# Performance work log

Measured on AMD Instinct MI355X. Metric: run time of the kernel, lower is better.

## Reference

```python
import jax, jax.numpy as jnp
import numpy as np

B = 16384
NUM_DENSE = 13
NUM_SPARSE = 26
VOCAB = 100000
EMB = 64
MLP_DIMS = [512, 256, 64]
TOP_OUT = 256
TRIU_I, TRIU_J = np.triu_indices(NUM_SPARSE, k=1)  # 325 pairs


def setup_inputs() -> dict:
    key = jax.random.key(0)
    ks = jax.random.split(key, 12)
    inp = {}
    inp["dense_features"] = jax.random.normal(ks[0], (B, NUM_DENSE), dtype=jnp.float32)
    inp["sparse_features"] = jax.random.randint(ks[1], (B, NUM_SPARSE), 0, VOCAB, dtype=jnp.int64)
    # embedding tables, all same shape -> stacked [F, V, D]
    inp["tables"] = jax.random.normal(ks[2], (NUM_SPARSE, VOCAB, EMB), dtype=jnp.float32) * 0.01
    # bottom (dense) MLP: 13 -> 512 -> 256 -> 64, weights stored [in, out]
    dims = [NUM_DENSE] + MLP_DIMS
    for li in range(3):
        fan_in = dims[li]
        inp[f"W{li}"] = jax.random.normal(ks[3 + li], (dims[li], dims[li + 1]), dtype=jnp.float32) / np.sqrt(fan_in)
        inp[f"b{li}"] = jnp.zeros((dims[li + 1],), dtype=jnp.float32)
    # top MLP: (64 + 325) -> 256
    top_in = MLP_DIMS[-1] + NUM_SPARSE * (NUM_SPARSE - 1) // 2
    inp["Wt"] = jax.random.normal(ks[6], (top_in, TOP_OUT), dtype=jnp.float32) / np.sqrt(top_in)
    inp["bt"] = jnp.zeros((TOP_OUT,), dtype=jnp.float32)
    return inp


def reference(dense_features, sparse_features, tables, W0, b0, W1, b1, W2, b2, Wt, bt):
    # bottom MLP with ReLU after every layer (as in the torch Sequential)
    x = jax.nn.relu(dense_features @ W0 + b0)
    x = jax.nn.relu(x @ W1 + b1)
    dense_out = jax.nn.relu(x @ W2 + b2)  # [B, 64]

    # embedding gather: table f indexed by sparse_features[:, f] -> [B, F, D]
    emb = jax.vmap(lambda t, idx: t[idx], in_axes=(0, 1), out_axes=1)(tables, sparse_features)

    # pairwise dot interaction, upper triangle (i < j) -> [B, 325]
    gram = jnp.einsum('bid,bjd->bij', emb, emb)
    interact = gram[:, TRIU_I, TRIU_J]

    features = jnp.concatenate([dense_out, interact], axis=1)  # [B, 389]
    return features @ Wt + bt  # [B, 256]
```

## Files before the change

kernel.cpp:

```cpp
#include <hip/hip_runtime.h>
#include <hip/hip_bf16.h>


#define BATCH   16384
#define NSPARSE 26
#define VOCAB   100000
#define EMB     64
#define KTOP    416
#define KREAL   389
#define SPB     32
#define ASTR    424
#define X1STR   520
#define X2STR   264

typedef __attribute__((ext_vector_type(8)))  short bf16x8;
typedef __attribute__((ext_vector_type(4)))  short s16x4;
typedef __attribute__((ext_vector_type(4)))  float f32x4;
typedef __attribute__((ext_vector_type(16))) float f32x16;

__device__ inline void gload_lds16(const void* g, void* l) {
    __builtin_amdgcn_global_load_lds(
        (const __attribute__((address_space(1))) void*)g,
        (__attribute__((address_space(3))) void*)l, 16, 0, 0);
}

__device__ inline short f2bf(float x) {
    __hip_bfloat16 h = __float2bfloat16(x);
    return *reinterpret_cast<short*>(&h);
}

__global__ __launch_bounds__(256)
void prep_weights(const float* __restrict__ W0, const float* __restrict__ W1,
                  const float* __restrict__ W2, const float* __restrict__ Wt,
                  short* __restrict__ W0t, short* __restrict__ W1t,
                  short* __restrict__ W2t, short* __restrict__ Wtt)
{
    __shared__ float tile[32][36];
    int b = blockIdx.x, t = threadIdx.x;
    const float* src; short* dst; int K, N, Kpad, k0, n0;
    if (b < 16)        {              src = W0; dst = W0t; K = 13;  N = 512; Kpad = 32;  k0 = 0;           n0 = b * 32; }
    else if (b < 144)  { int i = b - 16;  src = W1; dst = W1t; K = 512; N = 256; Kpad = 512; k0 = (i >> 3) * 32; n0 = (i & 7) * 32; }
    else if (b < 160)  { int i = b - 144; src = W2; dst = W2t; K = 256; N = 64;  Kpad = 256; k0 = (i >> 1) * 32; n0 = (i & 1) * 32; }
    else               { int i = b - 160; src = Wt; dst = Wtt; K = 389; N = 256; Kpad = 416; k0 = (i >> 3) * 32; n0 = (i & 7) * 32; }

    int r = t >> 3, c4 = (t & 7) * 4;
    int gr = k0 + r;
    float4 v = make_float4(0.f, 0.f, 0.f, 0.f);
    if (gr < K) v = *(const float4*)(src + (size_t)gr * N + n0 + c4);
    tile[r][c4 + 0] = v.x; tile[r][c4 + 1] = v.y;
    tile[r][c4 + 2] = v.z; tile[r][c4 + 3] = v.w;
    __syncthreads();
    s16x4 o;
    #pragma unroll
    for (int j = 0; j < 4; ++j) o[j] = f2bf(tile[c4 + j][r]);
    *(s16x4*)&dst[(size_t)(n0 + r) * Kpad + k0 + c4] = o;
}

__global__ __launch_bounds__(256, 2)
void fused_all(const int* __restrict__ sparse, const float* __restrict__ tables,
               const float* __restrict__ D,
               const short* __restrict__ W0t, const float* __restrict__ b0,
               const short* __restrict__ W1t, const float* __restrict__ b1,
               const short* __restrict__ W2t, const float* __restrict__ b2,
               const short* __restrict__ Wtt, const float* __restrict__ bt,
               float* __restrict__ out)
{
    __shared__ __align__(16) char smem[78848];
    short* As  = (short*)(smem);
    short* X1s = (short*)(smem + 27136);
    short* X2s = (short*)(smem + 27136);
    short* Bst = (short*)(smem + 60416);
    short* Ds  = (short*)(smem + 76800);

    int tid = threadIdx.x;
    int w = tid >> 6, lane = tid & 63;
    int lr = lane & 15, lg = lane >> 4;
    int wr = w >> 1, wc = w & 1;
    int swz = (lg ^ (lr & 3)) * 8;
    int sbase = blockIdx.x * SPB;

    for (int x = tid; x < SPB * 13; x += 256) {
        int r = x / 13, k = x - r * 13;
        Ds[r * 32 + k] = f2bf(D[(size_t)sbase * 13 + x]);
    }
    for (int x = tid; x < SPB * 19; x += 256) {
        int r = x / 19, k = 13 + (x - r * 19);
        Ds[r * 32 + k] = 0;
    }
    for (int x = tid; x < SPB * 27; x += 256) {
        int r = x / 27, c = x - r * 27;
        As[r * ASTR + KREAL + c] = 0;
    }
    __syncthreads();

    auto gram_phase = [&]() {
        int row = lane & 31, half = lane >> 5;
        int srow = (row < NSPARSE) ? row : 0;
        int idxv[8];
        #pragma unroll
        for (int li = 0; li < 8; ++li)
            idxv[li] = sparse[(sbase + w * 8 + li) * NSPARSE + srow];

        f32x4 Ca[4], Cb[4], Na[4], Nb[4];
        {
            const float* rp = tables + ((long)srow * VOCAB + idxv[0]) * EMB + half * 8;
            #pragma unroll
            for (int t = 0; t < 4; ++t) {
                Ca[t] = *(const f32x4*)(rp + t * 16);
                Cb[t] = *(const f32x4*)(rp + t * 16 + 4);
            }
        }
        #pragma unroll
        for (int li = 0; li < 8; ++li) {
            if (li < 7) {
                const float* rp = tables + ((long)srow * VOCAB + idxv[li + 1]) * EMB + half * 8;
                #pragma unroll
                for (int t = 0; t < 4; ++t) {
                    Na[t] = *(const f32x4*)(rp + t * 16);
                    Nb[t] = *(const f32x4*)(rp + t * 16 + 4);
                }
            }
            f32x16 acc = {};
            #pragma unroll
            for (int t = 0; t < 4; ++t) {
                bf16x8 f;
                #pragma unroll
                for (int j = 0; j < 4; ++j) f[j] = f2bf(Ca[t][j]);
                #pragma unroll
                for (int j = 0; j < 4; ++j) f[4 + j] = f2bf(Cb[t][j]);
                acc = __builtin_amdgcn_mfma_f32_32x32x16_bf16(f, f, acc, 0, 0, 0);
            }
            int c = row;
            if (c < NSPARSE) {
                #pragma unroll
                for (int reg = 0; reg < 16; ++reg) {
                    int r = (reg & 3) + 8 * (reg >> 2) + 4 * half;
                    if (r < c) {
                        int p = r * (2 * NSPARSE - r - 1) / 2 + (c - r - 1);
                        As[(w * 8 + li) * ASTR + 64 + p] = f2bf(acc[reg]);
                    }
                }
            }
            #pragma unroll
            for (int t = 0; t < 4; ++t) { Ca[t] = Na[t]; Cb[t] = Nb[t]; }
        }
    };

    auto mlp_phase = [&]() {
        {
            bf16x8 a = *(const bf16x8*)&Ds[(wr * 16 + lr) * 32 + lg * 8];
            f32x4 acc[16] = {};
            #pragma unroll
            for (int ni = 0; ni < 16; ++ni) {
                bf16x8 b = *(const bf16x8*)(W0t + (size_t)(wc * 256 + ni * 16 + lr) * 32 + lg * 8);
                acc[ni] = __builtin_amdgcn_mfma_f32_16x16x32_bf16(a, b, acc[ni], 0, 0, 0);
            }
            #pragma unroll
            for (int ni = 0; ni < 16; ++ni) {
                int col = wc * 256 + ni * 16 + lr;
                float bv = b0[col];
                #pragma unroll
                for (int j = 0; j < 4; ++j) {
                    int r = wr * 16 + lg * 4 + j;
                    X1s[r * X1STR + col] = f2bf(fmaxf(acc[ni][j] + bv, 0.f));
                }
            }
        }
        {
            f32x4 acc[8] = {};
            for (int k0 = 0; k0 < 512; k0 += 32) {
                #pragma unroll
                for (int rd = 0; rd < 4; ++rd) {
                    int slot = rd * 256 + tid;
                    int n = slot >> 2, kc = slot & 3;
                    gload_lds16(W1t + (size_t)n * 512 + k0 + (kc ^ (n & 3)) * 8, &Bst[slot * 8]);
                }
                __syncthreads();
                bf16x8 a = *(const bf16x8*)&X1s[(wr * 16 + lr) * X1STR + k0 + lg * 8];
                #pragma unroll
                for (int ni = 0; ni < 8; ++ni) {
                    int n = wc * 128 + ni * 16 + lr;
                    bf16x8 b = *(const bf16x8*)&Bst[n * 32 + swz];
                    acc[ni] = __builtin_amdgcn_mfma_f32_16x16x32_bf16(a, b, acc[ni], 0, 0, 0);
                }
                __syncthreads();
            }
            #pragma unroll
            for (int ni = 0; ni < 8; ++ni) {
                int col = wc * 128 + ni * 16 + lr;
                float bv = b1[col];
                #pragma unroll
                for (int j = 0; j < 4; ++j) {
                    int r = wr * 16 + lg * 4 + j;
                    X2s[r * X2STR + col] = f2bf(fmaxf(acc[ni][j] + bv, 0.f));
                }
            }
        }
        {
            f32x4 acc[2] = {};
            for (int k0 = 0; k0 < 256; k0 += 32) {
                {
                    int n = tid >> 2, kc = tid & 3;
                    gload_lds16(W2t + (size_t)n * 256 + k0 + (kc ^ (n & 3)) * 8, &Bst[tid * 8]);
                }
                __syncthreads();
                bf16x8 a = *(const bf16x8*)&X2s[(wr * 16 + lr) * X2STR + k0 + lg * 8];
                #pragma unroll
                for (int ni = 0; ni < 2; ++ni) {
                    int n = wc * 32 + ni * 16 + lr;
                    bf16x8 b = *(const bf16x8*)&Bst[n * 32 + swz];
                    acc[ni] = __builtin_amdgcn_mfma_f32_16x16x32_bf16(a, b, acc[ni], 0, 0, 0);
                }
                __syncthreads();
            }
            #pragma unroll
            for (int ni = 0; ni < 2; ++ni) {
                int col = wc * 32 + ni * 16 + lr;
                float bv = b2[col];
                #pragma unroll
                for (int j = 0; j < 4; ++j) {
                    int r = wr * 16 + lg * 4 + j;
                    As[r * ASTR + col] = f2bf(fmaxf(acc[ni][j] + bv, 0.f));
                }
            }
        }
    };

    if ((blockIdx.x >> 8) & 1) { mlp_phase(); gram_phase(); }
    else                       { gram_phase(); mlp_phase(); }

    {
        f32x4 acc[8] = {};
        for (int k0 = 0; k0 < KTOP; k0 += 32) {
            #pragma unroll
            for (int rd = 0; rd < 4; ++rd) {
                int slot = rd * 256 + tid;
                int n = slot >> 2, kc = slot & 3;
                gload_lds16(Wtt + (size_t)n * KTOP + k0 + (kc ^ (n & 3)) * 8, &Bst[slot * 8]);
            }
            __syncthreads();
            bf16x8 a = *(const bf16x8*)&As[(wr * 16 + lr) * ASTR + k0 + lg * 8];
            #pragma unroll
            for (int ni = 0; ni < 8; ++ni) {
                int n = wc * 128 + ni * 16 + lr;
                bf16x8 b = *(const bf16x8*)&Bst[n * 32 + swz];
                acc[ni] = __builtin_amdgcn_mfma_f32_16x16x32_bf16(a, b, acc[ni], 0, 0, 0);
            }
            __syncthreads();
        }
        #pragma unroll
        for (int ni = 0; ni < 8; ++ni) {
            int col = wc * 128 + ni * 16 + lr;
            float bv = bt[col];
            #pragma unroll
            for (int j = 0; j < 4; ++j) {
                int r = wr * 16 + lg * 4 + j;
                out[(size_t)(sbase + r) * 256 + col] = acc[ni][j] + bv;
            }
        }
    }
}

extern "C" void kernel_launch(void* const* d_in, const int* in_sizes, int n_in,
                              void* d_out, int out_size, void* d_ws, size_t ws_size,
                              hipStream_t stream)
{
    const float* dense  = (const float*)d_in[0];
    const int*   sparse = (const int*)  d_in[1];
    const float* tables = (const float*)d_in[2];
    const float* W0     = (const float*)d_in[3];
    const float* b0     = (const float*)d_in[4];
    const float* W1     = (const float*)d_in[5];
    const float* b1     = (const float*)d_in[6];
    const float* W2     = (const float*)d_in[7];
    const float* b2     = (const float*)d_in[8];
    const float* Wt     = (const float*)d_in[9];
    const float* bt     = (const float*)d_in[10];
    float* out = (float*)d_out;

    char* ws = (char*)d_ws;
    short* W0t = (short*)(ws);
    short* W1t = (short*)(ws + 32768);
    short* W2t = (short*)(ws + 294912);
    short* Wtt = (short*)(ws + 327680);

    prep_weights<<<264, 256, 0, stream>>>(W0, W1, W2, Wt, W0t, W1t, W2t, Wtt);

    fused_all<<<BATCH / SPB, 256, 0, stream>>>(sparse, tables, dense,
                                               W0t, b0, W1t, b1, W2t, b2,
                                               Wtt, bt, out);
}
```

Measured before the change: 52.03 us.

## Warp-specialize fused kernel: MLP waves overlap gather-gram waves, 64 samples per block

Moves from 256-thread blocks of 32 samples, where every wave ran the MLP and gram phases in sequence, to 512-thread blocks of 64 samples. Four waves run the bottom MLP while the other four gather embeddings and compute the gram interactions, so the MLP compute overlaps the gather latency. Each MLP wave now stages its own slice of the weights with its own waits instead of a block-wide barrier. LDS uses an XOR swizzle in place of padded strides, and the top GEMM double-buffers its weight tiles. The cost is one block per CU with about 156KB of LDS, and the gram work is split into 2/10/4-sample chunks to match the MLP stages, which may leave the two wave groups unbalanced.

```diff
diff --git a/kernel.cpp b/kernel.cpp
--- a/kernel.cpp
+++ b/kernel.cpp
@@ -5,13 +5,13 @@
 #define BATCH   16384
 #define NSPARSE 26
 #define VOCAB   100000
-#define EMB     64
 #define KTOP    416
 #define KREAL   389
-#define SPB     32
-#define ASTR    424
-#define X1STR   520
-#define X2STR   264
+#define SPB     64
+
+#define WAIT_VMCNT(N) asm volatile("s_waitcnt vmcnt(" #N ")" ::: "memory")
+#define WAIT_LGKM0()  asm volatile("s_waitcnt lgkmcnt(0)" ::: "memory")
+#define SBAR0() __builtin_amdgcn_sched_barrier(0)
 
 typedef __attribute__((ext_vector_type(8)))  short bf16x8;
 typedef __attribute__((ext_vector_type(4)))  short s16x4;
@@ -27,6 +27,19 @@
 __device__ inline short f2bf(float x) {
     __hip_bfloat16 h = __float2bfloat16(x);
     return *reinterpret_cast<short*>(&h);
+}
+
+__device__ inline f32x4 mfma16(bf16x8 a, bf16x8 b, f32x4 c) {
+    return __builtin_amdgcn_mfma_f32_16x16x32_bf16(a, b, c, 0, 0, 0);
+}
+
+__device__ inline short* ldsx2(char* base, int row, int ld, int col) {
+    int byte = ((row * ld + col) * 2) ^ ((row & 7) << 4);
+    return (short*)(base + byte);
+}
+__device__ inline bf16x8 ldsx16(const char* base, int row, int ld, int col) {
+    int byte = ((row * ld + col) * 2) ^ ((row & 7) << 4);
+    return *(const bf16x8*)(base + byte);
 }
 
 __global__ __launch_bounds__(256)
@@ -56,7 +69,63 @@
     *(s16x4*)&dst[(size_t)(n0 + r) * Kpad + k0 + c4] = o;
 }
 
-__global__ __launch_bounds__(256, 2)
+template<int CNT>
+__device__ void gram_run(int s0, int gw, int sbase,
+                         const int* __restrict__ sparse,
+                         const float* __restrict__ tables,
+                         char* AsG, int lane)
+{
+    int row = lane & 31, half = lane >> 5;
+    int srow = (row < NSPARSE) ? row : 0;
+    int sl0 = gw * 16 + s0;
+
+    const float* rp0 = tables + ((long)srow * VOCAB +
+        sparse[(sbase + sl0) * NSPARSE + srow]) * 64 + half * 8;
+    f32x4 Ca[4], Cb[4], Na[4], Nb[4];
+    #pragma unroll
+    for (int t = 0; t < 4; ++t) {
+        Ca[t] = *(const f32x4*)(rp0 + t * 16);
+        Cb[t] = *(const f32x4*)(rp0 + t * 16 + 4);
+    }
+    #pragma unroll
+    for (int li = 0; li < CNT; ++li) {
+        if (li + 1 < CNT) {
+            const float* rp = tables + ((long)srow * VOCAB +
+                sparse[(sbase + sl0 + li + 1) * NSPARSE + srow]) * 64 + half * 8;
+            #pragma unroll
+            for (int t = 0; t < 4; ++t) {
+                Na[t] = *(const f32x4*)(rp + t * 16);
+                Nb[t] = *(const f32x4*)(rp + t * 16 + 4);
+            }
+        }
+        f32x16 acc = {};
+        #pragma unroll
+        for (int t = 0; t < 4; ++t) {
+            bf16x8 f;
+            #pragma unroll
+            for (int j = 0; j < 4; ++j) f[j] = f2bf(Ca[t][j]);
+            #pragma unroll
+            for (int j = 0; j < 4; ++j) f[4 + j] = f2bf(Cb[t][j]);
+            acc = __builtin_amdgcn_mfma_f32_32x32x16_bf16(f, f, acc, 0, 0, 0);
+        }
+        int c = row, sl = sl0 + li;
+        if (c < NSPARSE) {
+            #pragma unroll
+            for (int reg = 0; reg < 16; ++reg) {
+                int r = (reg & 3) + 8 * (reg >> 2) + 4 * half;
+                if (r < c) {
+                    int p = r * (2 * NSPARSE - r - 1) / 2 + (c - r - 1);
+                    int byte = ((sl * 352 + p) * 2) ^ ((sl & 7) << 4);
+                    *(short*)(AsG + byte) = f2bf(acc[reg]);
+                }
+            }
+        }
+        #pragma unroll
+        for (int t = 0; t < 4; ++t) { Ca[t] = Na[t]; Cb[t] = Nb[t]; }
+    }
+}
+
+__global__ __launch_bounds__(512, 1)
 void fused_all(const int* __restrict__ sparse, const float* __restrict__ tables,
                const float* __restrict__ D,
                const short* __restrict__ W0t, const float* __restrict__ b0,
@@ -65,198 +134,186 @@
                const short* __restrict__ Wtt, const float* __restrict__ bt,
                float* __restrict__ out)
 {
-    __shared__ __align__(16) char smem[78848];
-    short* As  = (short*)(smem);
-    short* X1s = (short*)(smem + 27136);
-    short* X2s = (short*)(smem + 27136);
-    short* Bst = (short*)(smem + 60416);
-    short* Ds  = (short*)(smem + 76800);
+    __shared__ __align__(16) char smem[159744];
+    char* X1s  = smem;
+    char* AsD  = smem;
+    char* X2s  = smem + 65536;
+    char* AsG  = smem + 98304;
+    char* wbuf = smem + 143360;
 
     int tid = threadIdx.x;
     int w = tid >> 6, lane = tid & 63;
     int lr = lane & 15, lg = lane >> 4;
-    int wr = w >> 1, wc = w & 1;
-    int swz = (lg ^ (lr & 3)) * 8;
+    int swz8 = (lg ^ (lr & 3)) * 8;
     int sbase = blockIdx.x * SPB;
-
-    for (int x = tid; x < SPB * 13; x += 256) {
-        int r = x / 13, k = x - r * 13;
-        Ds[r * 32 + k] = f2bf(D[(size_t)sbase * 13 + x]);
-    }
-    for (int x = tid; x < SPB * 19; x += 256) {
-        int r = x / 19, k = 13 + (x - r * 19);
-        Ds[r * 32 + k] = 0;
-    }
-    for (int x = tid; x < SPB * 27; x += 256) {
-        int r = x / 27, c = x - r * 27;
-        As[r * ASTR + KREAL + c] = 0;
+    bool mlp = (w < 4);
+
+    if (mlp) {
+        bf16x8 a[4];
+        #pragma unroll
+        for (int mi = 0; mi < 4; ++mi) {
+            bf16x8 t = {};
+            if (lg < 2) {
+                #pragma unroll
+                for (int j = 0; j < 8; ++j) {
+                    int k = lg * 8 + j;
+                    if (k < 13)
+                        t[j] = f2bf(D[(size_t)(sbase + mi * 16 + lr) * 13 + k]);
+                }
+            }
+            a[mi] = t;
+        }
+        f32x4 acc[4][8] = {};
+        #pragma unroll
+        for (int ni = 0; ni < 8; ++ni) {
+            int n = w * 128 + ni * 16 + lr;
+            bf16x8 b = *(const bf16x8*)(W0t + (size_t)n * 32 + lg * 8);
+            #pragma unroll
+            for (int mi = 0; mi < 4; ++mi)
+                acc[mi][ni] = mfma16(a[mi], b, acc[mi][ni]);
+        }
+        #pragma unroll
+        for (int ni = 0; ni < 8; ++ni) {
+            int col = w * 128 + ni * 16 + lr;
+            float bv = b0[col];
+            #pragma unroll
+            for (int mi = 0; mi < 4; ++mi)
+                #pragma unroll
+                for (int j = 0; j < 4; ++j)
+                    *ldsx2(X1s, mi * 16 + lg * 4 + j, 512, col) =
+                        f2bf(fmaxf(acc[mi][ni][j] + bv, 0.f));
+        }
+    } else {
+        gram_run<2>(0, w - 4, sbase, sparse, tables, AsG, lane);
+        for (int x = lane; x < 16 * 27; x += 64) {
+            int sl = (w - 4) * 16 + x / 27, c = 325 + x % 27;
+            int byte = ((sl * 352 + c) * 2) ^ ((sl & 7) << 4);
+            *(short*)(AsG + byte) = 0;
+        }
     }
     __syncthreads();
 
-    auto gram_phase = [&]() {
-        int row = lane & 31, half = lane >> 5;
-        int srow = (row < NSPARSE) ? row : 0;
-        int idxv[8];
-        #pragma unroll
-        for (int li = 0; li < 8; ++li)
-            idxv[li] = sparse[(sbase + w * 8 + li) * NSPARSE + srow];
-
-        f32x4 Ca[4], Cb[4], Na[4], Nb[4];
-        {
-            const float* rp = tables + ((long)srow * VOCAB + idxv[0]) * EMB + half * 8;
-            #pragma unroll
-            for (int t = 0; t < 4; ++t) {
-                Ca[t] = *(const f32x4*)(rp + t * 16);
-                Cb[t] = *(const f32x4*)(rp + t * 16 + 4);
-            }
-        }
-        #pragma unroll
-        for (int li = 0; li < 8; ++li) {
-            if (li < 7) {
-                const float* rp = tables + ((long)srow * VOCAB + idxv[li + 1]) * EMB + half * 8;
-                #pragma unroll
-                for (int t = 0; t < 4; ++t) {
-                    Na[t] = *(const f32x4*)(rp + t * 16);
-                    Nb[t] = *(const f32x4*)(rp + t * 16 + 4);
-                }
-            }
-            f32x16 acc = {};
-            #pragma unroll
-            for (int t = 0; t < 4; ++t) {
-                bf16x8 f;
-                #pragma unroll
-                for (int j = 0; j < 4; ++j) f[j] = f2bf(Ca[t][j]);
-                #pragma unroll
-                for (int j = 0; j < 4; ++j) f[4 + j] = f2bf(Cb[t][j]);
-                acc = __builtin_amdgcn_mfma_f32_32x32x16_bf16(f, f, acc, 0, 0, 0);
-            }
-            int c = row;
-            if (c < NSPARSE) {
-                #pragma unroll
-                for (int reg = 0; reg < 16; ++reg) {
-                    int r = (reg & 3) + 8 * (reg >> 2) + 4 * half;
-                    if (r < c) {
-                        int p = r * (2 * NSPARSE - r - 1) / 2 + (c - r - 1);
-                        As[(w * 8 + li) * ASTR + 64 + p] = f2bf(acc[reg]);
-                    }
-                }
-            }
-            #pragma unroll
-            for (int t = 0; t < 4; ++t) { Ca[t] = Na[t]; Cb[t] = Nb[t]; }
-        }
-    };
-
-    auto mlp_phase = [&]() {
-        {
-            bf16x8 a = *(const bf16x8*)&Ds[(wr * 16 + lr) * 32 + lg * 8];
-            f32x4 acc[16] = {};
-            #pragma unroll
-            for (int ni = 0; ni < 16; ++ni) {
-                bf16x8 b = *(const bf16x8*)(W0t + (size_t)(wc * 256 + ni * 16 + lr) * 32 + lg * 8);
-                acc[ni] = __builtin_amdgcn_mfma_f32_16x16x32_bf16(a, b, acc[ni], 0, 0, 0);
-            }
-            #pragma unroll
-            for (int ni = 0; ni < 16; ++ni) {
-                int col = wc * 256 + ni * 16 + lr;
-                float bv = b0[col];
-                #pragma unroll
-                for (int j = 0; j < 4; ++j) {
-                    int r = wr * 16 + lg * 4 + j;
-                    X1s[r * X1STR + col] = f2bf(fmaxf(acc[ni][j] + bv, 0.f));
-                }
-            }
-        }
-        {
-            f32x4 acc[8] = {};
-            for (int k0 = 0; k0 < 512; k0 += 32) {
-                #pragma unroll
-                for (int rd = 0; rd < 4; ++rd) {
-                    int slot = rd * 256 + tid;
-                    int n = slot >> 2, kc = slot & 3;
-                    gload_lds16(W1t + (size_t)n * 512 + k0 + (kc ^ (n & 3)) * 8, &Bst[slot * 8]);
-                }
-                __syncthreads();
-                bf16x8 a = *(const bf16x8*)&X1s[(wr * 16 + lr) * X1STR + k0 + lg * 8];
-                #pragma unroll
-                for (int ni = 0; ni < 8; ++ni) {
-                    int n = wc * 128 + ni * 16 + lr;
-                    bf16x8 b = *(const bf16x8*)&Bst[n * 32 + swz];
-                    acc[ni] = __builtin_amdgcn_mfma_f32_16x16x32_bf16(a, b, acc[ni], 0, 0, 0);
-                }
-                __syncthreads();
-            }
-            #pragma unroll
-            for (int ni = 0; ni < 8; ++ni) {
-                int col = wc * 128 + ni * 16 + lr;
-                float bv = b1[col];
-                #pragma unroll
-                for (int j = 0; j < 4; ++j) {
-                    int r = wr * 16 + lg * 4 + j;
-                    X2s[r * X2STR + col] = f2bf(fmaxf(acc[ni][j] + bv, 0.f));
-                }
-            }
-        }
-        {
-            f32x4 acc[2] = {};
-            for (int k0 = 0; k0 < 256; k0 += 32) {
-                {
-                    int n = tid >> 2, kc = tid & 3;
-                    gload_lds16(W2t + (size_t)n * 256 + k0 + (kc ^ (n & 3)) * 8, &Bst[tid * 8]);
-                }
-                __syncthreads();
-                bf16x8 a = *(const bf16x8*)&X2s[(wr * 16 + lr) * X2STR + k0 + lg * 8];
-                #pragma unroll
-                for (int ni = 0; ni < 2; ++ni) {
-                    int n = wc * 32 + ni * 16 + lr;
-                    bf16x8 b = *(const bf16x8*)&Bst[n * 32 + swz];
-                    acc[ni] = __builtin_amdgcn_mfma_f32_16x16x32_bf16(a, b, acc[ni], 0, 0, 0);
-                }
-                __syncthreads();
+    if (mlp) {
+        char* buf = wbuf + w * 4096;
+        f32x4 acc[4][4] = {};
+        for (int k = 0; k < 16; ++k) {
+            int k0 = k * 32;
+            #pragma unroll
+            for (int it = 0; it < 4; ++it) {
+                int slot = it * 64 + lane;
+                int n = slot >> 2, kc = slot & 3;
+                gload_lds16(W1t + (size_t)(w * 64 + n) * 512 + k0 + (kc ^ (n & 3)) * 8,
+                            buf + slot * 16);
+            }
+            WAIT_VMCNT(0); SBAR0();
+            bf16x8 a[4];
+            #pragma unroll
+            for (int mi = 0; mi < 4; ++mi)
+                a[mi] = ldsx16(X1s, mi * 16 + lr, 512, k0 + lg * 8);
+            #pragma unroll
+            for (int ni = 0; ni < 4; ++ni) {
+                bf16x8 b = *(const bf16x8*)(buf + ((ni * 16 + lr) * 32 + swz8) * 2);
+                #pragma unroll
+                for (int mi = 0; mi < 4; ++mi)
+                    acc[mi][ni] = mfma16(a[mi], b, acc[mi][ni]);
+            }
+            WAIT_LGKM0(); SBAR0();
+        }
+        #pragma unroll
+        for (int ni = 0; ni < 4; ++ni) {
+            int col = w * 64 + ni * 16 + lr;
+            float bv = b1[col];
+            #pragma unroll
+            for (int mi = 0; mi < 4; ++mi)
+                #pragma unroll
+                for (int j = 0; j < 4; ++j)
+                    *ldsx2(X2s, mi * 16 + lg * 4 + j, 256, col) =
+                        f2bf(fmaxf(acc[mi][ni][j] + bv, 0.f));
+        }
+    } else {
+        gram_run<10>(2, w - 4, sbase, sparse, tables, AsG, lane);
+    }
+    __syncthreads();
+
+    if (mlp) {
+        char* buf = wbuf + w * 4096;
+        f32x4 acc[4] = {};
+        for (int k = 0; k < 8; ++k) {
+            int k0 = k * 32;
+            {
+                int n = lane >> 2, kc = lane & 3;
+                gload_lds16(W2t + (size_t)(w * 16 + n) * 256 + k0 + (kc ^ (n & 3)) * 8,
+                            buf + lane * 16);
+            }
+            WAIT_VMCNT(0); SBAR0();
+            bf16x8 b = *(const bf16x8*)(buf + (lr * 32 + swz8) * 2);
+            #pragma unroll
+            for (int mi = 0; mi < 4; ++mi) {
+                bf16x8 a = ldsx16(X2s, mi * 16 + lr, 256, k0 + lg * 8);
+                acc[mi] = mfma16(a, b, acc[mi]);
+            }
+            WAIT_LGKM0(); SBAR0();
+        }
+        int col = w * 16 + lr;
+        float bv = b2[col];
+        #pragma unroll
+        for (int mi = 0; mi < 4; ++mi)
+            #pragma unroll
+            for (int j = 0; j < 4; ++j)
+                *ldsx2(AsD, mi * 16 + lg * 4 + j, 64, col) =
+                    f2bf(fmaxf(acc[mi][j] + bv, 0.f));
+    } else {
+        gram_run<4>(12, w - 4, sbase, sparse, tables, AsG, lane);
+    }
+    __syncthreads();
+
+    {
+        char* bufA = X2s + w * 4096;
+        char* bufB = bufA + 2048;
+        auto stg = [&](char* dst, int k0) {
+            #pragma unroll
+            for (int it = 0; it < 2; ++it) {
+                int slot = it * 64 + lane;
+                int n = slot >> 2, kc = slot & 3;
+                gload_lds16(Wtt + (size_t)(w * 32 + n) * 416 + k0 + (kc ^ (n & 3)) * 8,
+                            dst + slot * 16);
+            }
+        };
+        stg(bufA, 0);
+        stg(bufB, 32);
+        f32x4 acc[4][2] = {};
+        for (int k = 0; k < 13; ++k) {
+            if (k < 11) { WAIT_VMCNT(2); } else { WAIT_VMCNT(0); }
+            SBAR0();
+            int k0 = k * 32;
+            char* buf = (k & 1) ? bufB : bufA;
+            bf16x8 a[4];
+            #pragma unroll
+            for (int mi = 0; mi < 4; ++mi) {
+                int r = mi * 16 + lr;
+                a[mi] = (k0 < 64) ? ldsx16(AsD, r, 64, k0 + lg * 8)
+                                  : ldsx16(AsG, r, 352, k0 - 64 + lg * 8);
             }
             #pragma unroll
             for (int ni = 0; ni < 2; ++ni) {
-                int col = wc * 32 + ni * 16 + lr;
-                float bv = b2[col];
-                #pragma unroll
-                for (int j = 0; j < 4; ++j) {
-                    int r = wr * 16 + lg * 4 + j;
-                    As[r * ASTR + col] = f2bf(fmaxf(acc[ni][j] + bv, 0.f));
-                }
-            }
-        }
-    };
-
-    if ((blockIdx.x >> 8) & 1) { mlp_phase(); gram_phase(); }
-    else                       { gram_phase(); mlp_phase(); }
-
-    {
-        f32x4 acc[8] = {};
-        for (int k0 = 0; k0 < KTOP; k0 += 32) {
-            #pragma unroll
-            for (int rd = 0; rd < 4; ++rd) {
-                int slot = rd * 256 + tid;
-                int n = slot >> 2, kc = slot & 3;
-                gload_lds16(Wtt + (size_t)n * KTOP + k0 + (kc ^ (n & 3)) * 8, &Bst[slot * 8]);
-            }
-            __syncthreads();
-            bf16x8 a = *(const bf16x8*)&As[(wr * 16 + lr) * ASTR + k0 + lg * 8];
-            #pragma unroll
-            for (int ni = 0; ni < 8; ++ni) {
-                int n = wc * 128 + ni * 16 + lr;
-                bf16x8 b = *(const bf16x8*)&Bst[n * 32 + swz];
-                acc[ni] = __builtin_amdgcn_mfma_f32_16x16x32_bf16(a, b, acc[ni], 0, 0, 0);
-            }
-            __syncthreads();
-        }
-        #pragma unroll
-        for (int ni = 0; ni < 8; ++ni) {
-            int col = wc * 128 + ni * 16 + lr;
+                bf16x8 b = *(const bf16x8*)(buf + ((ni * 16 + lr) * 32 + swz8) * 2);
+                #pragma unroll
+                for (int mi = 0; mi < 4; ++mi)
+                    acc[mi][ni] = mfma16(a[mi], b, acc[mi][ni]);
+            }
+            WAIT_LGKM0(); SBAR0();
+            if (k + 2 < 13) stg(buf, (k + 2) * 32);
+        }
+        #pragma unroll
+        for (int ni = 0; ni < 2; ++ni) {
+            int col = w * 32 + ni * 16 + lr;
             float bv = bt[col];
             #pragma unroll
-            for (int j = 0; j < 4; ++j) {
-                int r = wr * 16 + lg * 4 + j;
-                out[(size_t)(sbase + r) * 256 + col] = acc[ni][j] + bv;
-            }
+            for (int mi = 0; mi < 4; ++mi)
+                #pragma unroll
+                for (int j = 0; j < 4; ++j)
+                    out[(size_t)(sbase + mi * 16 + lg * 4 + j) * 256 + col] =
+                        acc[mi][ni][j] + bv;
         }
     }
 }
@@ -286,7 +343,7 @@
 
     prep_weights<<<264, 256, 0, stream>>>(W0, W1, W2, Wt, W0t, W1t, W2t, Wtt);
 
-    fused_all<<<BATCH / SPB, 256, 0, stream>>>(sparse, tables, dense,
+    fused_all<<<BATCH / SPB, 512, 0, stream>>>(sparse, tables, dense,
                                                W0t, b0, W1t, b1, W2t, b2,
                                                Wtt, bt, out);
 }
```

After: 45.91 us. 11.8% less time.
